# Performance work log

Hardware: AMD Instinct MI355X
Metric: run time of the kernel (lower is better)

## Reference

```python
import jax, jax.numpy as jnp
import numpy as np

EPS = 1e-5  # torch LayerNorm default

def layernorm(x, g, b):
    mu = jnp.mean(x, axis=-1, keepdims=True)
    var = jnp.mean(jnp.square(x - mu), axis=-1, keepdims=True)
    return (x - mu) * jax.lax.rsqrt(var + EPS) * g + b

def setup_inputs() -> dict:
    key = jax.random.key(0)
    ks = jax.random.split(key, 12)
    B, L1, L2 = 8, 2048, 2048
    D1, D2, E = 1024, 768, 1024
    s1, s2, se = D1 ** -0.5, D2 ** -0.5, E ** -0.5
    return {
        "modality1": jax.random.normal(ks[0], (B, L1, D1), jnp.float32),
        "modality2": jax.random.normal(ks[1], (B, L2, D2), jnp.float32),
        "ln1_g": jnp.ones((D1,), jnp.float32),
        "ln1_b": jnp.zeros((D1,), jnp.float32),
        "ln2_g": jnp.ones((D2,), jnp.float32),
        "ln2_b": jnp.zeros((D2,), jnp.float32),
        "Wq": jax.random.normal(ks[2], (D1, E), jnp.float32) * s1,
        "bq": jax.random.normal(ks[3], (E,), jnp.float32) * 0.01,
        "Wk": jax.random.normal(ks[4], (D2, E), jnp.float32) * s2,
        "bk": jax.random.normal(ks[5], (E,), jnp.float32) * 0.01,
        "Wv": jax.random.normal(ks[6], (D2, E), jnp.float32) * s2,
        "bv": jax.random.normal(ks[7], (E,), jnp.float32) * 0.01,
        "Wo": jax.random.normal(ks[8], (E, D1), jnp.float32) * se,
        "bo": jax.random.normal(ks[9], (D1,), jnp.float32) * 0.01,
    }

def reference(modality1, modality2, ln1_g, ln1_b, ln2_g, ln2_b,
              Wq, bq, Wk, bk, Wv, bv, Wo, bo):
    E = Wq.shape[1]
    scaling = E ** -0.5
    x1 = layernorm(modality1, ln1_g, ln1_b)   # [B, L1, D1]
    x2 = layernorm(modality2, ln2_g, ln2_b)   # [B, L2, D2]
    q = x1 @ Wq + bq                           # [B, L1, E]
    k = x2 @ Wk + bk                           # [B, L2, E]
    v = x2 @ Wv + bv                           # [B, L2, E]
    scores = jnp.einsum('bqe,bke->bqk', q, k) * scaling
    attn = jax.nn.softmax(scores, axis=-1)     # [B, L1, L2]
    ctx = jnp.einsum('bqk,bke->bqe', attn, v)  # [B, L1, E]
    return ctx @ Wo + bo                        # [B, L1, D1]
```

## Files before the change

kernel.cpp:

```cpp
#include <hip/hip_runtime.h>
#include <hip/hip_bf16.h>

typedef __bf16 bf16_t;
typedef __bf16 bf16x4_t __attribute__((ext_vector_type(4)));
typedef __bf16 bf16x8_t __attribute__((ext_vector_type(8)));
typedef float f32x4_t __attribute__((ext_vector_type(4)));
typedef float f32x16_t __attribute__((ext_vector_type(16)));

typedef __attribute__((address_space(1))) void gvoid_t;
typedef __attribute__((address_space(3))) void svoid_t;

__device__ __forceinline__ void gload_lds16(const void* g, void* s) {
    __builtin_amdgcn_global_load_lds((gvoid_t*)g, (svoid_t*)s, 16, 0, 0);
}

__device__ __forceinline__ void wg_barrier() {
    asm volatile("" ::: "memory");
    __builtin_amdgcn_s_barrier();
    asm volatile("" ::: "memory");
}

template <typename CT, bool BIAS, bool STORE_T = false>
__global__ __launch_bounds__(512, 2)
void gemm_bt(const bf16_t* __restrict__ A, const bf16_t* __restrict__ Bt,
             CT* __restrict__ C, const float* __restrict__ bias,
             int M, int N, int K, float scale,
             size_t sA, size_t sB, size_t sC, int tshift)
{
    __shared__ bf16_t As[4 * 256 * 32];
    __shared__ bf16_t Bs[4 * 256 * 32];

    const int nx = gridDim.x, ny = gridDim.y;
    const int nblk = nx * ny * (int)gridDim.z;
    int lin = blockIdx.x + nx * (blockIdx.y + ny * blockIdx.z);
    int tile = lin;
    if ((nblk & 7) == 0)
        tile = (lin & 7) * (nblk >> 3) + (lin >> 3);
    const int per_z = nx * ny;
    const int bz = tile / per_z;
    int t = tile - bz * per_z;
    const int SB = 8;
    const int band = t / (nx * SB);
    const int r = t - band * (nx * SB);
    const int h = min(SB, ny - band * SB);
    const int bx = r / h;
    const int by = band * SB + (r - bx * h);

    A  += (size_t)bz * sA;
    Bt += (size_t)bz * sB;
    C  += (size_t)bz * sC;

    const int tid  = threadIdx.x;
    const int wave = tid >> 6;
    const int lane = tid & 63;
    const int m0 = by * 256;
    const int n0 = bx * 256;

    const int rr = tid >> 2;
    const int cc = ((tid & 3) ^ ((rr >> 1) & 3)) * 8;
    const bf16_t* aw0 = A  + (size_t)(m0 + rr) * K + cc;
    const bf16_t* aw1 = aw0 + (size_t)128 * K;
    const bf16_t* bw0 = Bt + (size_t)(n0 + rr) * K + cc;
    const bf16_t* bw1 = bw0 + (size_t)128 * K;
    const int soff0 = wave * 512;
    const int soff1 = 4096 + wave * 512;

    const int wm = wave >> 2;
    const int wn = wave & 3;
    const int lr = lane & 31;
    const int kh = lane >> 5;
    const int swz = (lr >> 1) & 3;

    f32x16_t acc[4][2];
#pragma unroll
    for (int i = 0; i < 4; ++i)
#pragma unroll
        for (int j = 0; j < 2; ++j)
            acc[i][j] = (f32x16_t)(0.f);

    const int NT = K >> 5;

    auto stage = [&](int buf) {
        bf16_t* a = As + buf * 8192;
        bf16_t* b = Bs + buf * 8192;
        gload_lds16(aw0, a + soff0);
        gload_lds16(aw1, a + soff1);
        gload_lds16(bw0, b + soff0);
        gload_lds16(bw1, b + soff1);
        aw0 += 32; aw1 += 32; bw0 += 32; bw1 += 32;
    };

    stage(0);
    if (NT > 1) stage(1);
    if (NT > 2) stage(2);

    for (int j = 0; j < NT; ++j) {
        const int buf = j & 3;
        if (j + 3 < NT) {
            stage((j + 3) & 3);
            asm volatile("s_waitcnt vmcnt(12)" ::: "memory");
        } else if (j + 2 < NT) {
            asm volatile("s_waitcnt vmcnt(8)" ::: "memory");
        } else if (j + 1 < NT) {
            asm volatile("s_waitcnt vmcnt(4)" ::: "memory");
        } else {
            asm volatile("s_waitcnt vmcnt(0)" ::: "memory");
        }
        wg_barrier();

        const bf16_t* ab = As + buf * 8192;
        const bf16_t* bb = Bs + buf * 8192;
        bf16x8_t af[4][2], bfr[2][2];
#pragma unroll
        for (int mi = 0; mi < 4; ++mi)
#pragma unroll
            for (int kk = 0; kk < 2; ++kk)
                af[mi][kk] = *(const bf16x8_t*)
                    &ab[(wm * 128 + mi * 32 + lr) * 32 + ((2 * kk + kh) ^ swz) * 8];
#pragma unroll
        for (int nj = 0; nj < 2; ++nj)
#pragma unroll
            for (int kk = 0; kk < 2; ++kk)
                bfr[nj][kk] = *(const bf16x8_t*)
                    &bb[(wn * 64 + nj * 32 + lr) * 32 + ((2 * kk + kh) ^ swz) * 8];

        __builtin_amdgcn_s_setprio(1);
#pragma unroll
        for (int kk = 0; kk < 2; ++kk)
#pragma unroll
            for (int mi = 0; mi < 4; ++mi)
#pragma unroll
                for (int nj = 0; nj < 2; ++nj)
                    acc[mi][nj] = __builtin_amdgcn_mfma_f32_32x32x16_bf16(
                        af[mi][kk], bfr[nj][kk], acc[mi][nj], 0, 0, 0);
        __builtin_amdgcn_s_setprio(0);

        asm volatile("s_waitcnt lgkmcnt(0)" ::: "memory");
        wg_barrier();
    }

#pragma unroll
    for (int nj = 0; nj < 2; ++nj) {
        const int col = n0 + wn * 64 + nj * 32 + lr;
        const float bv = BIAS ? bias[col] : 0.0f;
#pragma unroll
        for (int mi = 0; mi < 4; ++mi) {
            f32x16_t v = acc[mi][nj];
#pragma unroll
            for (int g = 0; g < 4; ++g) {
                const int row = m0 + wm * 128 + mi * 32 + 8 * g + 4 * kh;
                if constexpr (STORE_T) {
                    const int b = row >> tshift;
                    const int l = row & ((1 << tshift) - 1);
                    bf16x4_t o;
#pragma unroll
                    for (int rr2 = 0; rr2 < 4; ++rr2)
                        o[rr2] = (bf16_t)(v[g * 4 + rr2] * scale + bv);
                    *(bf16x4_t*)((bf16_t*)C + ((size_t)b * N << tshift) +
                                 ((size_t)col << tshift) + l) = o;
                } else {
#pragma unroll
                    for (int rr2 = 0; rr2 < 4; ++rr2) {
                        float val = v[g * 4 + rr2] * scale + bv;
                        C[(size_t)(row + rr2) * N + col] = (CT)val;
                    }
                }
            }
        }
    }
}

template <int NV>
__global__ __launch_bounds__(256, 4)
void layernorm_k(const float* __restrict__ x, const float* __restrict__ g,
                 const float* __restrict__ b, bf16_t* __restrict__ y)
{
    const int D = NV * 256;
    const int wave = threadIdx.x >> 6, lane = threadIdx.x & 63;
    const size_t row = (size_t)blockIdx.x * 4 + wave;
    const float4* xr = (const float4*)(x + row * D);

    float4 v[NV];
    float s = 0.f, sq = 0.f;
#pragma unroll
    for (int i = 0; i < NV; ++i) {
        v[i] = xr[lane + 64 * i];
        s  += v[i].x + v[i].y + v[i].z + v[i].w;
        sq += v[i].x * v[i].x + v[i].y * v[i].y + v[i].z * v[i].z + v[i].w * v[i].w;
    }
#pragma unroll
    for (int m = 32; m; m >>= 1) {
        s  += __shfl_xor(s, m, 64);
        sq += __shfl_xor(sq, m, 64);
    }
    const float mean = s / D;
    const float rstd = rsqrtf(fmaxf(sq / D - mean * mean, 0.f) + 1e-5f);

#pragma unroll
    for (int i = 0; i < NV; ++i) {
        const int c4 = lane + 64 * i;
        float4 gg = ((const float4*)g)[c4];
        float4 bb = ((const float4*)b)[c4];
        bf16x4_t o;
        o[0] = (bf16_t)((v[i].x - mean) * rstd * gg.x + bb.x);
        o[1] = (bf16_t)((v[i].y - mean) * rstd * gg.y + bb.y);
        o[2] = (bf16_t)((v[i].z - mean) * rstd * gg.z + bb.z);
        o[3] = (bf16_t)((v[i].w - mean) * rstd * gg.w + bb.w);
        *(bf16x4_t*)(y + row * D + (size_t)c4 * 4) = o;
    }
}

__global__ __launch_bounds__(256, 4)
void softmax_rows(bf16_t* __restrict__ a)
{
    const int wave = threadIdx.x >> 6, lane = threadIdx.x & 63;
    const size_t row = (size_t)blockIdx.x * 4 + wave;
    bf16_t* r = a + row * 2048;

    float v[32];
    float mx = -3.0e38f;
#pragma unroll
    for (int i = 0; i < 4; ++i) {
        bf16x8_t t = *(const bf16x8_t*)(r + (size_t)(lane + 64 * i) * 8);
#pragma unroll
        for (int j = 0; j < 8; ++j) {
            v[i * 8 + j] = (float)t[j];
            mx = fmaxf(mx, v[i * 8 + j]);
        }
    }
#pragma unroll
    for (int m = 32; m; m >>= 1) mx = fmaxf(mx, __shfl_xor(mx, m, 64));
    float s = 0.f;
#pragma unroll
    for (int i = 0; i < 32; ++i) { v[i] = __expf(v[i] - mx); s += v[i]; }
#pragma unroll
    for (int m = 32; m; m >>= 1) s += __shfl_xor(s, m, 64);
    const float rs = 1.0f / s;
#pragma unroll
    for (int i = 0; i < 4; ++i) {
        bf16x8_t t;
#pragma unroll
        for (int j = 0; j < 8; ++j) t[j] = (bf16_t)(v[i * 8 + j] * rs);
        *(bf16x8_t*)(r + (size_t)(lane + 64 * i) * 8) = t;
    }
}

__global__ __launch_bounds__(256, 4)
void wconvT(const float* __restrict__ w, bf16_t* __restrict__ wt, int K, int N)
{
    __shared__ float s[32][33];
    const int tx = threadIdx.x, ty = threadIdx.y;
    const int n0 = blockIdx.x * 32, k0 = blockIdx.y * 32;
#pragma unroll
    for (int r = 0; r < 4; ++r)
        s[ty + r * 8][tx] = w[(size_t)(k0 + ty + r * 8) * N + n0 + tx];
    __syncthreads();
#pragma unroll
    for (int r = 0; r < 4; ++r)
        wt[(size_t)(n0 + ty + r * 8) * K + k0 + tx] = (bf16_t)s[tx][ty + r * 8];
}


extern "C" void kernel_launch(void* const* d_in, const int* in_sizes, int n_in,
                              void* d_out, int out_size, void* d_ws, size_t ws_size,
                              hipStream_t stream)
{
    const int B = 8, L1 = 2048, L2 = 2048, D1 = 1024, D2 = 768, E = 1024;
    const float scale = 0.03125f;
    const int tsh = 11;

    const float* m1   = (const float*)d_in[0];
    const float* m2   = (const float*)d_in[1];
    const float* ln1g = (const float*)d_in[2];
    const float* ln1b = (const float*)d_in[3];
    const float* ln2g = (const float*)d_in[4];
    const float* ln2b = (const float*)d_in[5];
    const float* Wq   = (const float*)d_in[6];
    const float* bq   = (const float*)d_in[7];
    const float* Wk   = (const float*)d_in[8];
    const float* bk   = (const float*)d_in[9];
    const float* Wv   = (const float*)d_in[10];
    const float* bv   = (const float*)d_in[11];
    const float* Wo   = (const float*)d_in[12];
    const float* bo   = (const float*)d_in[13];
    float* out = (float*)d_out;

    bf16_t* ws = (bf16_t*)d_ws;
    size_t off = 0;
    auto alloc = [&](size_t n) { bf16_t* p = ws + off; off += n; return p; };
    bf16_t* WqT = alloc((size_t)E * D1);
    bf16_t* WkT = alloc((size_t)E * D2);
    bf16_t* WvT = alloc((size_t)E * D2);
    bf16_t* WoT = alloc((size_t)D1 * E);
    bf16_t* x1  = alloc((size_t)B * L1 * D1);
    bf16_t* x2  = alloc((size_t)B * L2 * D2);
    bf16_t* Qb  = alloc((size_t)B * L1 * E);
    bf16_t* Kb  = alloc((size_t)B * L2 * E);
    bf16_t* VTb = alloc((size_t)B * E * L2);
    bf16_t* ctx = alloc((size_t)B * L1 * E);
    bf16_t* attn = ws + off;
    const bool batched = (off + (size_t)B * L1 * L2) * sizeof(bf16_t) <= ws_size;

    dim3 blk256(256);
    dim3 blk512(512);

    wconvT<<<dim3(E / 32, D1 / 32), dim3(32, 8), 0, stream>>>(Wq, WqT, D1, E);
    wconvT<<<dim3(E / 32, D2 / 32), dim3(32, 8), 0, stream>>>(Wk, WkT, D2, E);
    wconvT<<<dim3(E / 32, D2 / 32), dim3(32, 8), 0, stream>>>(Wv, WvT, D2, E);
    wconvT<<<dim3(D1 / 32, E / 32), dim3(32, 8), 0, stream>>>(Wo, WoT, E, D1);

    layernorm_k<4><<<dim3(B * L1 / 4), blk256, 0, stream>>>(m1, ln1g, ln1b, x1);
    layernorm_k<3><<<dim3(B * L2 / 4), blk256, 0, stream>>>(m2, ln2g, ln2b, x2);

    gemm_bt<bf16_t, true><<<dim3(E / 256, B * L1 / 256, 1), blk512, 0, stream>>>(
        x1, WqT, Qb, bq, B * L1, E, D1, 1.0f, 0, 0, 0, 0);
    gemm_bt<bf16_t, true><<<dim3(E / 256, B * L2 / 256, 1), blk512, 0, stream>>>(
        x2, WkT, Kb, bk, B * L2, E, D2, 1.0f, 0, 0, 0, 0);
    gemm_bt<bf16_t, true, true><<<dim3(E / 256, B * L2 / 256, 1), blk512, 0, stream>>>(
        x2, WvT, VTb, bv, B * L2, E, D2, 1.0f, 0, 0, 0, tsh);

    if (batched) {
        gemm_bt<bf16_t, false><<<dim3(L2 / 256, L1 / 256, B), blk512, 0, stream>>>(
            Qb, Kb, attn, nullptr, L1, L2, E, scale,
            (size_t)L1 * E, (size_t)L2 * E, (size_t)L1 * L2, 0);
        softmax_rows<<<dim3(B * L1 / 4), blk256, 0, stream>>>(attn);
        gemm_bt<bf16_t, false><<<dim3(E / 256, L1 / 256, B), blk512, 0, stream>>>(
            attn, VTb, ctx, nullptr, L1, E, L2, 1.0f,
            (size_t)L1 * L2, (size_t)E * L2, (size_t)L1 * E, 0);
    } else {
        for (int b = 0; b < B; ++b) {
            gemm_bt<bf16_t, false><<<dim3(L2 / 256, L1 / 256, 1), blk512, 0, stream>>>(
                Qb + (size_t)b * L1 * E, Kb + (size_t)b * L2 * E, attn, nullptr,
                L1, L2, E, scale, 0, 0, 0, 0);
            softmax_rows<<<dim3(L1 / 4), blk256, 0, stream>>>(attn);
            gemm_bt<bf16_t, false><<<dim3(E / 256, L1 / 256, 1), blk512, 0, stream>>>(
                attn, VTb + (size_t)b * E * L2, ctx + (size_t)b * L1 * E, nullptr,
                L1, E, L2, 1.0f, 0, 0, 0, 0);
        }
    }

    gemm_bt<float, true><<<dim3(D1 / 256, B * L1 / 256, 1), blk512, 0, stream>>>(
        ctx, WoT, out, bo, B * L1, D1, E, 1.0f, 0, 0, 0, 0);
}
```

Baseline: 573.1 us.

## Switch GEMM mainloop to K=64 double-buffered tiles with interleaved fragment loads

Replaces the 4-stage K=32 LDS pipeline with a 2-stage K=64 pipeline. LDS loads use a new 8-way XOR swizzle, and A/B fragment reads are split into sub-blocks interleaved with the MFMAs. The goal is to halve the number of barriers per K and lower register pressure for fragments. The cost is a shallower prefetch: each iteration waits on vmcnt(0), so global latency may be less well hidden.

```diff
diff --git a/kernel.cpp b/kernel.cpp
--- a/kernel.cpp
+++ b/kernel.cpp
@@ -27,8 +27,8 @@
              int M, int N, int K, float scale,
              size_t sA, size_t sB, size_t sC, int tshift)
 {
-    __shared__ bf16_t As[4 * 256 * 32];
-    __shared__ bf16_t Bs[4 * 256 * 32];
+    __shared__ bf16_t As[2 * 256 * 64];
+    __shared__ bf16_t Bs[2 * 256 * 64];
 
     const int nx = gridDim.x, ny = gridDim.y;
     const int nblk = nx * ny * (int)gridDim.z;
@@ -56,20 +56,18 @@
     const int m0 = by * 256;
     const int n0 = bx * 256;
 
-    const int rr = tid >> 2;
-    const int cc = ((tid & 3) ^ ((rr >> 1) & 3)) * 8;
-    const bf16_t* aw0 = A  + (size_t)(m0 + rr) * K + cc;
-    const bf16_t* aw1 = aw0 + (size_t)128 * K;
-    const bf16_t* bw0 = Bt + (size_t)(n0 + rr) * K + cc;
-    const bf16_t* bw1 = bw0 + (size_t)128 * K;
-    const int soff0 = wave * 512;
-    const int soff1 = 4096 + wave * 512;
+    const int srow = tid >> 3;
+    const int lc8  = ((tid & 7) ^ (srow & 7)) * 8;
+    const bf16_t* Ag = A  + (size_t)(m0 + srow) * K + lc8;
+    const bf16_t* Bg = Bt + (size_t)(n0 + srow) * K + lc8;
+    const size_t rs = (size_t)64 * K;
+    const int sbase = wave * 512;
 
     const int wm = wave >> 2;
     const int wn = wave & 3;
     const int lr = lane & 31;
     const int kh = lane >> 5;
-    const int swz = (lr >> 1) & 3;
+    const int rsw = lr & 7;
 
     f32x16_t acc[4][2];
 #pragma unroll
@@ -78,64 +76,69 @@
         for (int j = 0; j < 2; ++j)
             acc[i][j] = (f32x16_t)(0.f);
 
-    const int NT = K >> 5;
+    const int NT = K >> 6;
 
     auto stage = [&](int buf) {
-        bf16_t* a = As + buf * 8192;
-        bf16_t* b = Bs + buf * 8192;
-        gload_lds16(aw0, a + soff0);
-        gload_lds16(aw1, a + soff1);
-        gload_lds16(bw0, b + soff0);
-        gload_lds16(bw1, b + soff1);
-        aw0 += 32; aw1 += 32; bw0 += 32; bw1 += 32;
+        bf16_t* a = As + buf * 16384;
+        bf16_t* b = Bs + buf * 16384;
+        const bf16_t* ap = Ag;
+        const bf16_t* bp = Bg;
+#pragma unroll
+        for (int j = 0; j < 4; ++j) {
+            gload_lds16(ap, a + j * 4096 + sbase);
+            gload_lds16(bp, b + j * 4096 + sbase);
+            ap += rs; bp += rs;
+        }
+        Ag += 64; Bg += 64;
     };
 
     stage(0);
-    if (NT > 1) stage(1);
-    if (NT > 2) stage(2);
-
-    for (int j = 0; j < NT; ++j) {
-        const int buf = j & 3;
-        if (j + 3 < NT) {
-            stage((j + 3) & 3);
-            asm volatile("s_waitcnt vmcnt(12)" ::: "memory");
-        } else if (j + 2 < NT) {
-            asm volatile("s_waitcnt vmcnt(8)" ::: "memory");
-        } else if (j + 1 < NT) {
-            asm volatile("s_waitcnt vmcnt(4)" ::: "memory");
-        } else {
-            asm volatile("s_waitcnt vmcnt(0)" ::: "memory");
-        }
-        wg_barrier();
-
-        const bf16_t* ab = As + buf * 8192;
-        const bf16_t* bb = Bs + buf * 8192;
-        bf16x8_t af[4][2], bfr[2][2];
-#pragma unroll
-        for (int mi = 0; mi < 4; ++mi)
-#pragma unroll
-            for (int kk = 0; kk < 2; ++kk)
-                af[mi][kk] = *(const bf16x8_t*)
-                    &ab[(wm * 128 + mi * 32 + lr) * 32 + ((2 * kk + kh) ^ swz) * 8];
-#pragma unroll
-        for (int nj = 0; nj < 2; ++nj)
-#pragma unroll
-            for (int kk = 0; kk < 2; ++kk)
-                bfr[nj][kk] = *(const bf16x8_t*)
-                    &bb[(wn * 64 + nj * 32 + lr) * 32 + ((2 * kk + kh) ^ swz) * 8];
-
-        __builtin_amdgcn_s_setprio(1);
-#pragma unroll
-        for (int kk = 0; kk < 2; ++kk)
-#pragma unroll
-            for (int mi = 0; mi < 4; ++mi)
-#pragma unroll
-                for (int nj = 0; nj < 2; ++nj)
-                    acc[mi][nj] = __builtin_amdgcn_mfma_f32_32x32x16_bf16(
-                        af[mi][kk], bfr[nj][kk], acc[mi][nj], 0, 0, 0);
-        __builtin_amdgcn_s_setprio(0);
-
-        asm volatile("s_waitcnt lgkmcnt(0)" ::: "memory");
+    asm volatile("s_waitcnt vmcnt(0)" ::: "memory");
+    wg_barrier();
+
+    for (int kt = 0; kt < NT; ++kt) {
+        const int buf = kt & 1;
+        if (kt + 1 < NT) stage(buf ^ 1);
+
+        const bf16_t* ab = As + buf * 16384;
+        const bf16_t* bb = Bs + buf * 16384;
+
+#pragma unroll
+        for (int kp = 0; kp < 2; ++kp) {
+            bf16x8_t bfr[2][2];
+#pragma unroll
+            for (int nj = 0; nj < 2; ++nj)
+#pragma unroll
+                for (int kq = 0; kq < 2; ++kq)
+                    bfr[nj][kq] = *(const bf16x8_t*)
+                        &bb[(wn * 64 + nj * 32 + lr) * 64 +
+                            (((kp * 2 + kq) * 2 + kh) ^ rsw) * 8];
+#pragma unroll
+            for (int mp = 0; mp < 2; ++mp) {
+                bf16x8_t af[2][2];
+#pragma unroll
+                for (int mq = 0; mq < 2; ++mq)
+#pragma unroll
+                    for (int kq = 0; kq < 2; ++kq)
+                        af[mq][kq] = *(const bf16x8_t*)
+                            &ab[(wm * 128 + (mp * 2 + mq) * 32 + lr) * 64 +
+                                (((kp * 2 + kq) * 2 + kh) ^ rsw) * 8];
+                __builtin_amdgcn_s_setprio(1);
+#pragma unroll
+                for (int mq = 0; mq < 2; ++mq)
+#pragma unroll
+                    for (int nj = 0; nj < 2; ++nj)
+#pragma unroll
+                        for (int kq = 0; kq < 2; ++kq)
+                            acc[mp * 2 + mq][nj] =
+                                __builtin_amdgcn_mfma_f32_32x32x16_bf16(
+                                    af[mq][kq], bfr[nj][kq],
+                                    acc[mp * 2 + mq][nj], 0, 0, 0);
+                __builtin_amdgcn_s_setprio(0);
+            }
+        }
+
+        asm volatile("s_waitcnt vmcnt(0) lgkmcnt(0)" ::: "memory");
         wg_barrier();
     }
 
```

After: 514.5 us. 1.11x faster.
